# Optimization experiments

Hardware: AMD Instinct MI355X
Metric: run time of the kernel (lower is better)

The kernel has to match this reference:

```python
import jax, jax.numpy as jnp
import numpy as np

N, K, D = 32768, 8192, 512
COMMITMENT_COST = 0.25

def setup_inputs() -> dict:
    key = jax.random.key(0)
    k1, k2 = jax.random.split(key)
    z = jax.random.normal(k1, (N, D), dtype=jnp.float32)
    # original inits uniform(-1/K, 1/K); scaled uniform keeps same distribution
    emb_weight = jax.random.uniform(k2, (K, D), dtype=jnp.float32, minval=-1.0 / K, maxval=1.0 / K)
    return {"z": z, "emb_weight": emb_weight}

def reference(z, emb_weight):
    z_flat = z.reshape(-1, emb_weight.shape[1])  # [N, D]
    # squared L2 distances: ||z||^2 + ||e||^2 - 2 z e^T  -> [N, K]
    distances = (
        jnp.sum(z_flat ** 2, axis=1, keepdims=True)
        + jnp.sum(emb_weight ** 2, axis=1)
        - 2.0 * jnp.matmul(z_flat, emb_weight.T)
    )
    code_indices = jnp.argmin(distances, axis=1)  # [N]
    quantized = emb_weight[code_indices]          # [N, D] gather
    e_latent_loss = jnp.mean((jax.lax.stop_gradient(quantized) - z_flat) ** 2)
    q_latent_loss = jnp.mean((quantized - jax.lax.stop_gradient(z_flat)) ** 2)
    loss = q_latent_loss + COMMITMENT_COST * e_latent_loss
    # straight-through estimator
    quantized_st = z_flat + jax.lax.stop_gradient(quantized - z_flat)
    return quantized_st, loss, code_indices
```

## Files before the change

kernel.cpp:

```cpp
#include <hip/hip_runtime.h>


#define N_ROWS 32768
#define K_CODES 8192
#define DIM 512

typedef __attribute__((ext_vector_type(8))) short short8;
typedef __attribute__((ext_vector_type(4))) float f32x4;

#define MARGIN 5e-4f

__device__ __forceinline__ unsigned short f2bf(float f) {
  unsigned int u = __float_as_uint(f);
  u = u + 0x7fffu + ((u >> 16) & 1u);
  return (unsigned short)(u >> 16);
}

__device__ __forceinline__ double shfl_xor_dbl(double v, int m) {
  union { double d; int i[2]; } u;
  u.d = v;
  u.i[0] = __shfl_xor(u.i[0], m, 64);
  u.i[1] = __shfl_xor(u.i[1], m, 64);
  return u.d;
}

__device__ __forceinline__ float opaque_f(float x) {
  asm volatile("" : "+v"(x));
  return x;
}

__global__ __launch_bounds__(256) void cvtnorm_k(const float* __restrict__ in,
                                                 unsigned short* __restrict__ outb,
                                                 float* __restrict__ outn) {
  const int r = blockIdx.x * 4 + (threadIdx.x >> 6);
  const int lane = threadIdx.x & 63;
  const float* xr = in + (size_t)r * DIM + lane * 8;
  const float4 a = *(const float4*)xr;
  const float4 b = *(const float4*)(xr + 4);
  uint4 o;
  o.x = (unsigned)f2bf(a.x) | ((unsigned)f2bf(a.y) << 16);
  o.y = (unsigned)f2bf(a.z) | ((unsigned)f2bf(a.w) << 16);
  o.z = (unsigned)f2bf(b.x) | ((unsigned)f2bf(b.y) << 16);
  o.w = (unsigned)f2bf(b.z) | ((unsigned)f2bf(b.w) << 16);
  *(uint4*)(outb + (size_t)r * DIM + lane * 8) = o;
  double s = (double)a.x * a.x + (double)a.y * a.y + (double)a.z * a.z + (double)a.w * a.w
           + (double)b.x * b.x + (double)b.y * b.y + (double)b.z * b.z + (double)b.w * b.w;
#pragma unroll
  for (int m = 1; m < 64; m <<= 1) s += shfl_xor_dbl(s, m);
  if (lane == 0) outn[r] = (float)s;
}

__global__ __launch_bounds__(512, 4) void gemm_topk(
    const unsigned short* __restrict__ A,
    const unsigned short* __restrict__ B,
    const float* __restrict__ en2,
    float* __restrict__ candk,
    int* __restrict__ candi)
{
  __shared__ char lds[69120];
  float* scorebuf = (float*)lds;
  float* e2s = (float*)(lds + 68608);

  const int tid = threadIdx.x;
  const int lane = tid & 63, wave = tid >> 6;
  const int wm = wave >> 1, wn = wave & 1;
  const int quad = lane >> 4, lcol = lane & 15;
  const int bx = blockIdx.x >> 3, by = blockIdx.x & 7;
  const int row0 = bx * 256;
  const int cstart = by * 1024;
  const int hf = tid & 1, srow = tid >> 1;

  float tk0 = 3.4e38f, tk1 = 3.4e38f, tk2 = 3.4e38f, tk3 = 3.4e38f;
  int ti0 = 0, ti1 = 0, ti2 = 0, ti3 = 0;

  const int srw = lane >> 3;
  const int sch = (lane & 7) ^ srw;
  const unsigned short* Ag =
      A + ((size_t)(row0 + wave * 32 + srw)) * DIM + sch * 8;
  const int ldsA = wave * 4096;
  const int ldsB = 32768 + wave * 2048;

  const int xr = lcol & 7;
  int abase[4], bbase[4];
#pragma unroll
  for (int i = 0; i < 4; ++i) abase[i] = (wm * 64 + i * 16 + lcol) * 128;
#pragma unroll
  for (int j = 0; j < 4; ++j) bbase[j] = 32768 + (wn * 64 + j * 16 + lcol) * 128;
  int coff[2];
#pragma unroll
  for (int kk = 0; kk < 2; ++kk) coff[kk] = ((kk * 4 + quad) ^ xr) * 16;

#pragma unroll 1
  for (int ct = 0; ct < 8; ++ct) {
    const int c0 = cstart + ct * 128;
    if (tid < 128) e2s[tid] = en2[c0 + tid];
    const unsigned short* Bg =
        B + ((size_t)(c0 + wave * 16 + srw)) * DIM + sch * 8;

    f32x4 acc[4][4];
#pragma unroll
    for (int i = 0; i < 4; ++i)
#pragma unroll
      for (int j = 0; j < 4; ++j) acc[i][j] = 0.f;

#pragma unroll
    for (int kt = 0; kt < 8; ++kt) {
      const int k0 = kt * 64;
      __syncthreads();
#pragma unroll
      for (int j = 0; j < 4; ++j) {
        __builtin_amdgcn_global_load_lds(
            (const __attribute__((address_space(1))) void*)(uintptr_t)(Ag + k0 + j * (8 * DIM)),
            (__attribute__((address_space(3))) void*)(uintptr_t)(lds + ldsA + j * 1024),
            16, 0, 0);
      }
#pragma unroll
      for (int j = 0; j < 2; ++j) {
        __builtin_amdgcn_global_load_lds(
            (const __attribute__((address_space(1))) void*)(uintptr_t)(Bg + k0 + j * (8 * DIM)),
            (__attribute__((address_space(3))) void*)(uintptr_t)(lds + ldsB + j * 1024),
            16, 0, 0);
      }
      __syncthreads();
#pragma unroll
      for (int kk = 0; kk < 2; ++kk) {
        short8 af[4], bfr[4];
#pragma unroll
        for (int i = 0; i < 4; ++i) af[i] = *(const short8*)(lds + abase[i] + coff[kk]);
#pragma unroll
        for (int j = 0; j < 4; ++j) bfr[j] = *(const short8*)(lds + bbase[j] + coff[kk]);
#pragma unroll
        for (int i = 0; i < 4; ++i)
#pragma unroll
          for (int j = 0; j < 4; ++j)
            acc[i][j] = __builtin_amdgcn_mfma_f32_16x16x32_bf16(af[i], bfr[j], acc[i][j], 0, 0, 0);
      }
    }

#pragma unroll 1
    for (int h = 0; h < 2; ++h) {
      __syncthreads();
      if (wn == h) {
#pragma unroll
        for (int i = 0; i < 4; ++i)
#pragma unroll
          for (int j = 0; j < 4; ++j) {
            const float eb2 = e2s[64 * h + 16 * j + lcol];
#pragma unroll
            for (int r = 0; r < 4; ++r)
              scorebuf[(wm * 64 + i * 16 + quad * 4 + r) * 67 + 16 * j + lcol] =
                  fmaf(acc[i][j][r], -2.0f, eb2);
          }
      }
      __syncthreads();
      const float* sp = scorebuf + srow * 67 + hf * 32;
      const int idbase = c0 + 64 * h + 32 * hf;
#pragma unroll 8
      for (int cc = 0; cc < 32; ++cc) {
        const float key = sp[cc];
        if (key < tk3) {
          const int id = idbase + cc;
          if (key < tk2) {
            tk3 = tk2; ti3 = ti2;
            if (key < tk1) {
              tk2 = tk1; ti2 = ti1;
              if (key < tk0) { tk1 = tk0; ti1 = ti0; tk0 = key; ti0 = id; }
              else           { tk1 = key; ti1 = id; }
            } else { tk2 = key; ti2 = id; }
          } else { tk3 = key; ti3 = id; }
        }
      }
    }
  }

  const size_t cb = ((size_t)(row0 + srow)) * 64 + by * 8 + hf * 4;
  candk[cb + 0] = tk0; candk[cb + 1] = tk1; candk[cb + 2] = tk2; candk[cb + 3] = tk3;
  candi[cb + 0] = ti0; candi[cb + 1] = ti1; candi[cb + 2] = ti2; candi[cb + 3] = ti3;
}

__global__ __launch_bounds__(256) void rescore_np(
    const float* __restrict__ z, const float* __restrict__ e,
    const float* __restrict__ a32, const float* __restrict__ b32,
    const float* __restrict__ candk, const int* __restrict__ candi,
    float* __restrict__ idxout)
{
  const int row = blockIdx.x * 4 + (threadIdx.x >> 6);
  const int lane = threadIdx.x & 63;

  const float myk = candk[(size_t)row * 64 + lane];
  float kmin = myk;
#pragma unroll
  for (int m = 1; m < 64; m <<= 1) kmin = fminf(kmin, __shfl_xor(kmin, m, 64));
  const float cut = kmin + MARGIN;

  float bd = 3.4e38f;
  int bc = 0x7fffffff;
  if (myk <= cut) {
    const int c = candi[(size_t)row * 64 + lane];
    const float* zr = z + (size_t)row * DIM;
    const float* er = e + (size_t)c * DIM;
    float s = 0.0f;
#pragma unroll 4
    for (int k4 = 0; k4 < 96; ++k4) {
      const float4 zv = *(const float4*)(zr + k4 * 4);
      const float4 ev = *(const float4*)(er + k4 * 4);
      s = fmaf(zv.x, ev.x, s);
      s = fmaf(zv.y, ev.y, s);
      s = fmaf(zv.z, ev.z, s);
      s = fmaf(zv.w, ev.w, s);
    }
    const float cA = s;
    s = 0.0f;
#pragma unroll 4
    for (int k4 = 96; k4 < 128; ++k4) {
      const float4 zv = *(const float4*)(zr + k4 * 4);
      const float4 ev = *(const float4*)(er + k4 * 4);
      s = fmaf(zv.x, ev.x, s);
      s = fmaf(zv.y, ev.y, s);
      s = fmaf(zv.z, ev.z, s);
      s = fmaf(zv.w, ev.w, s);
    }
    const float m = cA + s;
    const float t1 = a32[row] + b32[c];
    const float t2 = opaque_f(2.0f * m);
    bd = t1 - t2;
    bc = c;
  }
#pragma unroll
  for (int mm = 1; mm < 64; mm <<= 1) {
    const float od = __shfl_xor(bd, mm, 64);
    const int oc = __shfl_xor(bc, mm, 64);
    if (od < bd || (od == bd && oc < bc)) { bd = od; bc = oc; }
  }
  if (lane == 0) idxout[row] = (float)bc;
}

__global__ __launch_bounds__(256) void writeout_k(
    const float* __restrict__ z, const float* __restrict__ e,
    const float* __restrict__ idxf, float* __restrict__ outq,
    double* __restrict__ accum)
{
  const int tid = threadIdx.x;
  double s = 0.0;
  size_t gid = (size_t)blockIdx.x * 256 + tid;
#pragma unroll 1
  for (int it = 0; it < 16; ++it, gid += 262144) {
    const int row = (int)(gid >> 7);
    const int dq = ((int)gid & 127) << 2;
    const int c = (int)idxf[row];
    const float4 q4 = *(const float4*)(e + (size_t)c * DIM + dq);
    const float4 z4 = *(const float4*)(z + (size_t)row * DIM + dq);
    const float tx = q4.x - z4.x, ty = q4.y - z4.y, tz = q4.z - z4.z, tw = q4.w - z4.w;
    float4 o;
    o.x = z4.x + tx; o.y = z4.y + ty; o.z = z4.z + tz; o.w = z4.w + tw;
    *(float4*)(outq + (size_t)row * DIM + dq) = o;
    s += (double)tx * tx + (double)ty * ty + (double)tz * tz + (double)tw * tw;
  }
#pragma unroll
  for (int m = 1; m < 64; m <<= 1) s += shfl_xor_dbl(s, m);
  __shared__ double wsum[4];
  if ((tid & 63) == 0) wsum[tid >> 6] = s;
  __syncthreads();
  if (tid == 0) atomicAdd(accum, wsum[0] + wsum[1] + wsum[2] + wsum[3]);
}

__global__ void finalize_k(const double* __restrict__ accum, float* __restrict__ lossp) {
  *lossp = (float)(1.25 * accum[0] / (double)((size_t)N_ROWS * DIM));
}

extern "C" void kernel_launch(void* const* d_in, const int* in_sizes, int n_in,
                              void* d_out, int out_size, void* d_ws, size_t ws_size,
                              hipStream_t stream) {
  const float* z = (const float*)d_in[0];
  const float* e = (const float*)d_in[1];
  float* out = (float*)d_out;
  char* ob = (char*)d_out;

  unsigned short* zb = (unsigned short*)ob;
  unsigned short* eb = (unsigned short*)(ob + 33554432);
  float* b32   = (float*)(ob + 41943040);
  float* a32   = (float*)(ob + 41975808);
  float* candk = (float*)(ob + 42106880);
  int*   candi = (int*)(ob + 50495488);

  float* lossp = out + 16777216;
  float* idxs  = out + 16777217;
  double* accum = (double*)d_ws;

  hipMemsetAsync(d_ws, 0, sizeof(double), stream);
  cvtnorm_k<<<8192, 256, 0, stream>>>(z, zb, a32);
  cvtnorm_k<<<2048, 256, 0, stream>>>(e, eb, b32);
  gemm_topk<<<1024, 512, 0, stream>>>(zb, eb, b32, candk, candi);
  rescore_np<<<8192, 256, 0, stream>>>(z, e, a32, b32, candk, candi, idxs);
  writeout_k<<<1024, 256, 0, stream>>>(z, e, idxs, out, accum);
  finalize_k<<<1, 1, 0, stream>>>(accum, lossp);
}
```

Measured before the change: 944.6 us.

## Triple-buffer GEMM K-loop with async global-to-LDS prefetch and preload codebook norms

```diff
diff --git a/kernel.cpp b/kernel.cpp
--- a/kernel.cpp
+++ b/kernel.cpp
@@ -57,9 +57,9 @@
     float* __restrict__ candk,
     int* __restrict__ candi)
 {
-  __shared__ char lds[69120];
+  __shared__ char lds[77824];
   float* scorebuf = (float*)lds;
-  float* e2s = (float*)(lds + 68608);
+  float* e2sAll = (float*)(lds + 73728);
 
   const int tid = threadIdx.x;
   const int lane = tid & 63, wave = tid >> 6;
@@ -70,32 +70,57 @@
   const int cstart = by * 1024;
   const int hf = tid & 1, srow = tid >> 1;
 
+  e2sAll[tid] = en2[cstart + tid];
+  e2sAll[tid + 512] = en2[cstart + 512 + tid];
+
   float tk0 = 3.4e38f, tk1 = 3.4e38f, tk2 = 3.4e38f, tk3 = 3.4e38f;
   int ti0 = 0, ti1 = 0, ti2 = 0, ti3 = 0;
 
-  const int srw = lane >> 3;
-  const int sch = (lane & 7) ^ srw;
+  const int schm = (lane & 3) ^ ((lane >> 3) & 3);
   const unsigned short* Ag =
-      A + ((size_t)(row0 + wave * 32 + srw)) * DIM + sch * 8;
-  const int ldsA = wave * 4096;
-  const int ldsB = 32768 + wave * 2048;
-
-  const int xr = lcol & 7;
-  int abase[4], bbase[4];
-#pragma unroll
-  for (int i = 0; i < 4; ++i) abase[i] = (wm * 64 + i * 16 + lcol) * 128;
-#pragma unroll
-  for (int j = 0; j < 4; ++j) bbase[j] = 32768 + (wn * 64 + j * 16 + lcol) * 128;
-  int coff[2];
-#pragma unroll
-  for (int kk = 0; kk < 2; ++kk) coff[kk] = ((kk * 4 + quad) ^ xr) * 16;
+      A + ((size_t)(row0 + wave * 32 + (lane >> 2))) * DIM + schm * 8;
+  const int dstA = wave * 2048;
+  const int dstB = 16384 + wave * 1024;
+
+  const int swz = (quad ^ ((lcol >> 1) & 3)) * 16;
+  int aoff[4], boff[4];
+#pragma unroll
+  for (int i = 0; i < 4; ++i) aoff[i] = (wm * 64 + i * 16 + lcol) * 64 + swz;
+#pragma unroll
+  for (int j = 0; j < 4; ++j) boff[j] = 16384 + (wn * 64 + j * 16 + lcol) * 64 + swz;
+
+#define ASGP const __attribute__((address_space(1))) void*
+#define LDSP __attribute__((address_space(3))) void*
+#define STAGE(ktv, bb) do {                                                        \
+    const unsigned short* As_ = Ag + (ktv) * 32;                                   \
+    const unsigned short* Bs_ = Bg + (ktv) * 32;                                   \
+    __builtin_amdgcn_global_load_lds((ASGP)(uintptr_t)(As_),                       \
+        (LDSP)(uintptr_t)(lds + (bb) + dstA), 16, 0, 0);                           \
+    __builtin_amdgcn_global_load_lds((ASGP)(uintptr_t)(As_ + 16 * DIM),            \
+        (LDSP)(uintptr_t)(lds + (bb) + dstA + 1024), 16, 0, 0);                    \
+    __builtin_amdgcn_global_load_lds((ASGP)(uintptr_t)(Bs_),                       \
+        (LDSP)(uintptr_t)(lds + (bb) + dstB), 16, 0, 0);                           \
+  } while (0)
+
+#define COMPUTE(cbb) do {                                                          \
+    short8 af[4], bv[4];                                                           \
+    _Pragma("unroll")                                                              \
+    for (int i = 0; i < 4; ++i) af[i] = *(const short8*)(lds + (cbb) + aoff[i]);   \
+    _Pragma("unroll")                                                              \
+    for (int j = 0; j < 4; ++j) bv[j] = *(const short8*)(lds + (cbb) + boff[j]);   \
+    _Pragma("unroll")                                                              \
+    for (int i = 0; i < 4; ++i)                                                    \
+      _Pragma("unroll")                                                            \
+      for (int j = 0; j < 4; ++j)                                                  \
+        acc[i][j] = __builtin_amdgcn_mfma_f32_16x16x32_bf16(af[i], bv[j],          \
+                                                            acc[i][j], 0, 0, 0);   \
+  } while (0)
 
 #pragma unroll 1
   for (int ct = 0; ct < 8; ++ct) {
     const int c0 = cstart + ct * 128;
-    if (tid < 128) e2s[tid] = en2[c0 + tid];
     const unsigned short* Bg =
-        B + ((size_t)(c0 + wave * 16 + srw)) * DIM + sch * 8;
+        B + ((size_t)(c0 + wave * 16 + (lane >> 2))) * DIM + schm * 8;
 
     f32x4 acc[4][4];
 #pragma unroll
@@ -103,39 +128,25 @@
 #pragma unroll
       for (int j = 0; j < 4; ++j) acc[i][j] = 0.f;
 
-#pragma unroll
-    for (int kt = 0; kt < 8; ++kt) {
-      const int k0 = kt * 64;
-      __syncthreads();
-#pragma unroll
-      for (int j = 0; j < 4; ++j) {
-        __builtin_amdgcn_global_load_lds(
-            (const __attribute__((address_space(1))) void*)(uintptr_t)(Ag + k0 + j * (8 * DIM)),
-            (__attribute__((address_space(3))) void*)(uintptr_t)(lds + ldsA + j * 1024),
-            16, 0, 0);
-      }
-#pragma unroll
-      for (int j = 0; j < 2; ++j) {
-        __builtin_amdgcn_global_load_lds(
-            (const __attribute__((address_space(1))) void*)(uintptr_t)(Bg + k0 + j * (8 * DIM)),
-            (__attribute__((address_space(3))) void*)(uintptr_t)(lds + ldsB + j * 1024),
-            16, 0, 0);
-      }
-      __syncthreads();
-#pragma unroll
-      for (int kk = 0; kk < 2; ++kk) {
-        short8 af[4], bfr[4];
-#pragma unroll
-        for (int i = 0; i < 4; ++i) af[i] = *(const short8*)(lds + abase[i] + coff[kk]);
-#pragma unroll
-        for (int j = 0; j < 4; ++j) bfr[j] = *(const short8*)(lds + bbase[j] + coff[kk]);
-#pragma unroll
-        for (int i = 0; i < 4; ++i)
-#pragma unroll
-          for (int j = 0; j < 4; ++j)
-            acc[i][j] = __builtin_amdgcn_mfma_f32_16x16x32_bf16(af[i], bfr[j], acc[i][j], 0, 0, 0);
-      }
+    __syncthreads();
+    STAGE(0, 0);
+    STAGE(1, 24576);
+    int cb = 0, nb = 24576, fb = 49152;
+#pragma unroll 1
+    for (int kt = 0; kt < 15; ++kt) {
+      asm volatile("s_waitcnt vmcnt(3)" ::: "memory");
+      __builtin_amdgcn_s_barrier();
+      asm volatile("" ::: "memory");
+      __builtin_amdgcn_sched_barrier(0);
+      if (kt < 14) STAGE(kt + 2, fb);
+      COMPUTE(cb);
+      const int t = cb; cb = nb; nb = fb; fb = t;
     }
+    asm volatile("s_waitcnt vmcnt(0)" ::: "memory");
+    __builtin_amdgcn_s_barrier();
+    asm volatile("" ::: "memory");
+    __builtin_amdgcn_sched_barrier(0);
+    COMPUTE(cb);
 
 #pragma unroll 1
     for (int h = 0; h < 2; ++h) {
@@ -145,7 +156,7 @@
         for (int i = 0; i < 4; ++i)
 #pragma unroll
           for (int j = 0; j < 4; ++j) {
-            const float eb2 = e2s[64 * h + 16 * j + lcol];
+            const float eb2 = e2sAll[ct * 128 + 64 * h + 16 * j + lcol];
 #pragma unroll
             for (int r = 0; r < 4; ++r)
               scorebuf[(wm * 64 + i * 16 + quad * 4 + r) * 67 + 16 * j + lcol] =
@@ -173,9 +184,9 @@
     }
   }
 
-  const size_t cb = ((size_t)(row0 + srow)) * 64 + by * 8 + hf * 4;
-  candk[cb + 0] = tk0; candk[cb + 1] = tk1; candk[cb + 2] = tk2; candk[cb + 3] = tk3;
-  candi[cb + 0] = ti0; candi[cb + 1] = ti1; candi[cb + 2] = ti2; candi[cb + 3] = ti3;
+  const size_t cb2 = ((size_t)(row0 + srow)) * 64 + by * 8 + hf * 4;
+  candk[cb2 + 0] = tk0; candk[cb2 + 1] = tk1; candk[cb2 + 2] = tk2; candk[cb2 + 3] = tk3;
+  candi[cb2 + 0] = ti0; candi[cb2 + 1] = ti1; candi[cb2 + 2] = ti2; candi[cb2 + 3] = ti3;
 }
 
 __global__ __launch_bounds__(256) void rescore_np(
```

After: 788.2 us. 16.6% less time.
